# Optimization experiments

Measured on AMD Instinct MI355X. Metric: run time of the kernel, lower is better.

The kernel has to match this reference:

```python
import jax, jax.numpy as jnp
import numpy as np

B, T, D = 2, 2048, 1024
H, HD = 16, 64  # num_heads, num_hiddens_per_head


def setup_inputs() -> dict:
    key = jax.random.key(0)
    ks = jax.random.split(key, 6)
    scale = 1.0 / np.sqrt(D)
    inputs_q = jax.random.normal(ks[0], (B, T, D), dtype=jnp.float32)
    inputs_kv = jax.random.normal(ks[1], (B, T, D), dtype=jnp.float32)
    # causal mask, broadcastable to [b, h, t, T]
    mask = jnp.tril(jnp.ones((T, T), dtype=bool))[None, None, :, :]
    Wq = jax.random.normal(ks[2], (D, H * HD), dtype=jnp.float32) * scale
    Wk = jax.random.normal(ks[3], (D, H * HD), dtype=jnp.float32) * scale
    Wv = jax.random.normal(ks[4], (D, H * HD), dtype=jnp.float32) * scale
    Wo = jax.random.normal(ks[5], (H * HD, D), dtype=jnp.float32) * scale
    return {"inputs_q": inputs_q, "inputs_kv": inputs_kv, "mask": mask,
            "Wq": Wq, "Wk": Wk, "Wv": Wv, "Wo": Wo}


def reference(inputs_q, inputs_kv, mask, Wq, Wk, Wv, Wo):
    b, t, _ = inputs_q.shape
    q = (inputs_q @ Wq).reshape(b, -1, H, HD)
    k = (inputs_kv @ Wk).reshape(b, -1, H, HD)
    v = (inputs_kv @ Wv).reshape(b, -1, H, HD)
    scores = jnp.einsum('bthd,bThd->bhtT', q, k) * (1.0 / jnp.sqrt(HD))
    scores = jnp.where(mask, scores, jnp.finfo(jnp.float32).min)
    attn = jax.nn.softmax(scores, axis=-1)
    out = jnp.einsum('bhtT,bThd->bthd', attn, v).reshape(b, t, H * HD)
    return out @ Wo
```

## Files before the change

### kernel.cpp

```cpp
#include <hip/hip_runtime.h>
#include <hip/hip_bf16.h>

#define B_  2
#define T_  2048
#define D_  1024
#define H_  16
#define HD_ 64

typedef __bf16 bf16x8 __attribute__((ext_vector_type(8)));
typedef float  f32x4  __attribute__((ext_vector_type(4)));

#define MFIX 8.0f

__device__ __forceinline__ __bf16 f2b(float f) {
  __hip_bfloat16 h = __float2bfloat16(f);
  return *reinterpret_cast<__bf16*>(&h);
}

__device__ __forceinline__ void gload_lds16(const __bf16* g, __bf16* l) {
  __builtin_amdgcn_global_load_lds((const unsigned int*)g, (unsigned int*)l, 16, 0, 0);
}

__global__ __launch_bounds__(256) void prep_k(const float* __restrict__ Xq,
                                              const float* __restrict__ Xkv,
                                              const float* __restrict__ Wq,
                                              const float* __restrict__ Wk,
                                              const float* __restrict__ Wv,
                                              const float* __restrict__ Wo,
                                              __hip_bfloat16* __restrict__ Xq_b,
                                              __hip_bfloat16* __restrict__ Xkv_b,
                                              __hip_bfloat16* __restrict__ WTall,
                                              __hip_bfloat16* __restrict__ WoT) {
  const int blk = blockIdx.x;
  if (blk < 8192) {
    const float* x = (blk < 4096) ? Xq : Xkv;
    __hip_bfloat16* y = (blk < 4096) ? Xq_b : Xkv_b;
    const size_t i = ((size_t)(blk & 4095) * 256 + threadIdx.x) * 4;
    f32x4 v = *(const f32x4*)(x + i);
    union { ushort4 u; __hip_bfloat16 h[4]; } o;
#pragma unroll
    for (int j = 0; j < 4; ++j) o.h[j] = __float2bfloat16(v[j]);
    *(ushort4*)(y + i) = o.u;
    return;
  }
  __shared__ float tile[64][65];
  const int wid  = (blk - 8192) >> 8;
  const int tid_ = (blk - 8192) & 255;
  const float* in = (wid == 0) ? Wq : (wid == 1) ? Wk : (wid == 2) ? Wv : Wo;
  __hip_bfloat16* out = (wid == 3) ? WoT : (WTall + (size_t)wid * 1024 * D_);
  const int bx = (tid_ & 15) * 64, by = (tid_ >> 4) * 64;
  const int tx = threadIdx.x & 63, ty = threadIdx.x >> 6;
#pragma unroll
  for (int i = ty; i < 64; i += 4)
    tile[i][tx] = in[(size_t)(by + i) * D_ + bx + tx];
  __syncthreads();
#pragma unroll
  for (int i = ty; i < 64; i += 4)
    out[(size_t)(bx + i) * D_ + by + tx] = __float2bfloat16(tile[tx][i]);
}

__global__ __launch_bounds__(256) void vtrans_k(const __hip_bfloat16* __restrict__ in,
                                                __hip_bfloat16* __restrict__ out) {
  __shared__ __hip_bfloat16 tl[64][65];
  const int bh = blockIdx.y;
  const int t0 = blockIdx.x * 64;
  const int tx = threadIdx.x & 63, ty = threadIdx.x >> 6;
  const __hip_bfloat16* src = in + (size_t)bh * T_ * HD_;
  __hip_bfloat16* dst = out + (size_t)bh * HD_ * T_;
#pragma unroll
  for (int i = ty; i < 64; i += 4)
    tl[i][tx] = src[(size_t)(t0 + i) * HD_ + tx];
  __syncthreads();
#pragma unroll
  for (int i = ty; i < 64; i += 4)
    dst[(size_t)i * T_ + t0 + tx] = tl[tx][i];
}

__global__ __launch_bounds__(256) void gemm_qkv_k(const __bf16* __restrict__ Aq,
                                                  const __bf16* __restrict__ Akv,
                                                  const __bf16* __restrict__ WTall,
                                                  __hip_bfloat16* __restrict__ Qd,
                                                  __hip_bfloat16* __restrict__ Kd,
                                                  __hip_bfloat16* __restrict__ Vd) {
  __shared__ __align__(16) __bf16 Al[128 * 32];
  __shared__ __align__(16) __bf16 Bl[128 * 32];

  const int bm = blockIdx.x * 128;
  const int bn = blockIdx.y * 128;
  const int w  = bn >> 10;
  const __bf16* A = (w == 0) ? Aq : Akv;

  const int wave = threadIdx.x >> 6, lane = threadIdx.x & 63;
  const int wm = (wave >> 1) * 64, wn = (wave & 1) * 64;
  const int lo = lane & 15, qh = lane >> 4;

  const int srow = threadIdx.x >> 2;
  const int skc  = (threadIdx.x & 3) * 8;
  const __bf16* Ag0 = A      + (size_t)(bm + srow) * D_ + skc;
  const __bf16* Bg0 = WTall  + (size_t)(bn + srow) * D_ + skc;
  __bf16* Al0 = Al + threadIdx.x * 8;
  __bf16* Bl0 = Bl + threadIdx.x * 8;

  f32x4 acc[4][4] = {};

  for (int k0 = 0; k0 < D_; k0 += 32) {
    __syncthreads();
    gload_lds16(Ag0 + k0,           Al0);
    gload_lds16(Ag0 + 64 * D_ + k0, Al0 + 64 * 32);
    gload_lds16(Bg0 + k0,           Bl0);
    gload_lds16(Bg0 + 64 * D_ + k0, Bl0 + 64 * 32);
    __syncthreads();

    bf16x8 af[4], bfr[4];
#pragma unroll
    for (int mt = 0; mt < 4; ++mt)
      af[mt] = *(const bf16x8*)(Al + (wm + mt * 16 + lo) * 32 + qh * 8);
#pragma unroll
    for (int nt = 0; nt < 4; ++nt)
      bfr[nt] = *(const bf16x8*)(Bl + (wn + nt * 16 + lo) * 32 + qh * 8);
#pragma unroll
    for (int mt = 0; mt < 4; ++mt)
#pragma unroll
      for (int nt = 0; nt < 4; ++nt)
        acc[mt][nt] = __builtin_amdgcn_mfma_f32_16x16x32_bf16(af[mt], bfr[nt], acc[mt][nt], 0, 0, 0);
  }

  __hip_bfloat16* dst = (w == 0) ? Qd : (w == 1) ? Kd : Vd;
  const float scale = (w == 0) ? 0.125f : 1.0f;
  const int col0 = (bn + wn) & 1023;
#pragma unroll
  for (int mt = 0; mt < 4; ++mt)
#pragma unroll
    for (int nt = 0; nt < 4; ++nt)
#pragma unroll
      for (int r = 0; r < 4; ++r) {
        const int m = bm + wm + mt * 16 + 4 * qh + r;
        const int n = col0 + nt * 16 + lo;
        const int b = m >> 11, t = m & (T_ - 1);
        const int h = n >> 6,  d = n & 63;
        dst[(((size_t)(b * H_ + h) * T_ + t) << 6) + d] =
            __float2bfloat16(acc[mt][nt][r] * scale);
      }
}

__global__ __launch_bounds__(256) void gemm_out_k(const __bf16* __restrict__ A,
                                                  const __bf16* __restrict__ Bt,
                                                  float* __restrict__ C) {
  __shared__ __align__(16) __bf16 Al[128 * 32];
  __shared__ __align__(16) __bf16 Bl[64 * 32];

  const int bm = blockIdx.x * 128;
  const int bn = blockIdx.y * 64;
  const int wave = threadIdx.x >> 6, lane = threadIdx.x & 63;
  const int wm = (wave >> 1) * 64, wn = (wave & 1) * 32;
  const int lo = lane & 15, qh = lane >> 4;

  const int srow = threadIdx.x >> 2;
  const int skc  = (threadIdx.x & 3) * 8;
  const __bf16* Ag0 = A  + (size_t)(bm + srow) * D_ + skc;
  const __bf16* Bg0 = Bt + (size_t)(bn + srow) * D_ + skc;
  __bf16* Al0 = Al + threadIdx.x * 8;
  __bf16* Bl0 = Bl + threadIdx.x * 8;

  f32x4 acc[4][2] = {};

  for (int k0 = 0; k0 < D_; k0 += 32) {
    __syncthreads();
    gload_lds16(Ag0 + k0,           Al0);
    gload_lds16(Ag0 + 64 * D_ + k0, Al0 + 64 * 32);
    gload_lds16(Bg0 + k0,           Bl0);
    __syncthreads();

    bf16x8 af[4], bfr[2];
#pragma unroll
    for (int mt = 0; mt < 4; ++mt)
      af[mt] = *(const bf16x8*)(Al + (wm + mt * 16 + lo) * 32 + qh * 8);
#pragma unroll
    for (int nt = 0; nt < 2; ++nt)
      bfr[nt] = *(const bf16x8*)(Bl + (wn + nt * 16 + lo) * 32 + qh * 8);
#pragma unroll
    for (int mt = 0; mt < 4; ++mt)
#pragma unroll
      for (int nt = 0; nt < 2; ++nt)
        acc[mt][nt] = __builtin_amdgcn_mfma_f32_16x16x32_bf16(af[mt], bfr[nt], acc[mt][nt], 0, 0, 0);
  }

#pragma unroll
  for (int mt = 0; mt < 4; ++mt)
#pragma unroll
    for (int nt = 0; nt < 2; ++nt)
#pragma unroll
      for (int r = 0; r < 4; ++r) {
        const int m = bm + wm + mt * 16 + 4 * qh + r;
        const int n = bn + wn + nt * 16 + lo;
        C[(size_t)m * D_ + n] = acc[mt][nt][r];
      }
}

__global__ __launch_bounds__(256) void attn_slice_k(const __hip_bfloat16* __restrict__ Q,
                                                    const __hip_bfloat16* __restrict__ K,
                                                    const __hip_bfloat16* __restrict__ Vt,
                                                    float* __restrict__ Ppart) {
  __shared__ __align__(16) __bf16 Kl[64 * 64];
  __shared__ __align__(16) __bf16 Vl[64 * 64];
  __shared__ __align__(16) __bf16 Pl[4][16][72];

  const int bh = blockIdx.x;
  const int u  = blockIdx.y;
  int qb, sl;
  if (u < 8)       { qb = u;                    sl = 0; }
  else if (u < 24) { qb = 8  + ((u - 8) >> 1);  sl = (u - 8) & 1; }
  else if (u < 48) { qb = 16 + (u - 24) / 3;    sl = (u - 24) % 3; }
  else             { qb = 24 + ((u - 48) >> 2); sl = (u - 48) & 3; }
  const int jt0 = sl * 8;
  const int jt_end = (jt0 + 8 < qb + 1) ? jt0 + 8 : qb + 1;
  const int t0 = qb * 64;

  const int wave = threadIdx.x >> 6, lane = threadIdx.x & 63;
  const int lo = lane & 15, qh = lane >> 4;

  const __hip_bfloat16* Qb = Q  + (size_t)bh * T_ * HD_;
  const __bf16* Kb = (const __bf16*)(K  + (size_t)bh * T_ * HD_);
  const __bf16* Vb = (const __bf16*)(Vt + (size_t)bh * HD_ * T_);

  const int srow = threadIdx.x >> 3;
  const int ssc  = (threadIdx.x & 7) ^ (srow & 7);
  __bf16* Kd0 = Kl + threadIdx.x * 8;
  __bf16* Kd1 = Kl + 2048 + threadIdx.x * 8;
  __bf16* Vd0 = Vl + threadIdx.x * 8;
  __bf16* Vd1 = Vl + 2048 + threadIdx.x * 8;

  bf16x8 qf[2];
  qf[0] = *(const bf16x8*)(Qb + (size_t)(t0 + wave * 16 + lo) * HD_ + qh * 8);
  qf[1] = *(const bf16x8*)(Qb + (size_t)(t0 + wave * 16 + lo) * HD_ + 32 + qh * 8);

  const int rc0 = (qh)     ^ (lo & 7);
  const int rc1 = (4 + qh) ^ (lo & 7);

  f32x4 o[4] = {};
  float lp[4] = {0.f, 0.f, 0.f, 0.f};

  for (int jt = jt0; jt < jt_end; ++jt) {
    const int jb = jt * 64;
    const bool diag = (jt == qb);

    __syncthreads();
    gload_lds16(Kb + (size_t)(jb + srow)      * HD_ + ssc * 8, Kd0);
    gload_lds16(Kb + (size_t)(jb + 32 + srow) * HD_ + ssc * 8, Kd1);
    gload_lds16(Vb + (size_t)srow        * T_ + jb + ssc * 8, Vd0);
    gload_lds16(Vb + (size_t)(32 + srow) * T_ + jb + ssc * 8, Vd1);
    __syncthreads();

    f32x4 s[4];
#pragma unroll
    for (int nt = 0; nt < 4; ++nt) {
      if (diag && nt > wave) { s[nt] = (f32x4){-1e30f, -1e30f, -1e30f, -1e30f}; continue; }
      f32x4 acc = {0.f, 0.f, 0.f, 0.f};
      bf16x8 kf0 = *(const bf16x8*)(Kl + (nt * 16 + lo) * 64 + rc0 * 8);
      acc = __builtin_amdgcn_mfma_f32_16x16x32_bf16(qf[0], kf0, acc, 0, 0, 0);
      bf16x8 kf1 = *(const bf16x8*)(Kl + (nt * 16 + lo) * 64 + rc1 * 8);
      acc = __builtin_amdgcn_mfma_f32_16x16x32_bf16(qf[1], kf1, acc, 0, 0, 0);
      if (diag && nt == wave) {
#pragma unroll
        for (int r = 0; r < 4; ++r)
          if (lo > 4 * qh + r) acc[r] = -1e30f;
      }
      s[nt] = acc;
    }

#pragma unroll
    for (int nt = 0; nt < 4; ++nt)
#pragma unroll
      for (int r = 0; r < 4; ++r) {
        const float p = __expf(s[nt][r] - MFIX);
        lp[r] += p;
        Pl[wave][4 * qh + r][nt * 16 + lo] = f2b(p);
      }

#pragma unroll
    for (int ks = 0; ks < 2; ++ks) {
      bf16x8 pf = *(const bf16x8*)&Pl[wave][lo][ks * 32 + qh * 8];
      const int rc = ks ? rc1 : rc0;
#pragma unroll
      for (int nt = 0; nt < 4; ++nt) {
        bf16x8 vf = *(const bf16x8*)(Vl + (nt * 16 + lo) * 64 + rc * 8);
        o[nt] = __builtin_amdgcn_mfma_f32_16x16x32_bf16(pf, vf, o[nt], 0, 0, 0);
      }
    }
  }

#pragma unroll
  for (int r = 0; r < 4; ++r)
#pragma unroll
    for (int msk = 1; msk < 16; msk <<= 1)
      lp[r] += __shfl_xor(lp[r], msk, 64);

  float* base = Ppart + (size_t)(bh * 80 + u) * 64 * 65 + (size_t)wave * 16 * 65;
#pragma unroll
  for (int nt = 0; nt < 4; ++nt)
#pragma unroll
    for (int r = 0; r < 4; ++r)
      base[(4 * qh + r) * 65 + nt * 16 + lo] = o[nt][r];
  if (lo == 0) {
#pragma unroll
    for (int r = 0; r < 4; ++r)
      base[(4 * qh + r) * 65 + 64] = lp[r];
  }
}

__global__ __launch_bounds__(256) void attn_combine_k(const float* __restrict__ Ppart,
                                                      __hip_bfloat16* __restrict__ O) {
  const int bh = blockIdx.x, qb = blockIdx.y;
  const int ns = (qb >> 3) + 1;
  const int ubase = (qb < 8) ? qb
                  : (qb < 16) ? 8 + 2 * (qb - 8)
                  : (qb < 24) ? 24 + 3 * (qb - 16)
                  : 48 + 4 * (qb - 24);
  const int d = threadIdx.x & 63, r0 = threadIdx.x >> 6;
  const int b = bh >> 4, h = bh & 15;
  const float* ub = Ppart + (size_t)(bh * 80 + ubase) * 64 * 65;

  for (int row = r0; row < 64; row += 4) {
    float acc = 0.f, l = 0.f;
    for (int s = 0; s < ns; ++s) {
      acc += ub[(size_t)s * 64 * 65 + row * 65 + d];
      l   += ub[(size_t)s * 64 * 65 + row * 65 + 64];
    }
    const int t = qb * 64 + row;
    O[((size_t)(b * T_ + t) << 10) + h * 64 + d] = __float2bfloat16(acc / l);
  }
}

extern "C" void kernel_launch(void* const* d_in, const int* in_sizes, int n_in,
                              void* d_out, int out_size, void* d_ws, size_t ws_size,
                              hipStream_t stream) {
  const float* Xq  = (const float*)d_in[0];
  const float* Xkv = (const float*)d_in[1];
  const float* Wq  = (const float*)d_in[3];
  const float* Wk  = (const float*)d_in[4];
  const float* Wv  = (const float*)d_in[5];
  const float* Wo  = (const float*)d_in[6];

  char* ws = (char*)d_ws;
  const size_t MB = 1024ull * 1024ull;
  __hip_bfloat16* WTall = (__hip_bfloat16*)(ws + 0 * MB);
  __hip_bfloat16* WoT   = (__hip_bfloat16*)(ws + 6 * MB);
  __hip_bfloat16* Qw    = (__hip_bfloat16*)(ws + 8 * MB);
  __hip_bfloat16* Kw    = (__hip_bfloat16*)(ws + 16 * MB);
  __hip_bfloat16* Vw    = (__hip_bfloat16*)(ws + 24 * MB);
  __hip_bfloat16* AO    = (__hip_bfloat16*)(ws + 32 * MB);
  float*          Ppart = (float*)        (ws + 40 * MB);
  __hip_bfloat16* Xq_b  = (__hip_bfloat16*)(ws + 84 * MB);
  __hip_bfloat16* Xkv_b = (__hip_bfloat16*)(ws + 92 * MB);

  const dim3 tb(256);

  prep_k<<<dim3(9216), tb, 0, stream>>>(Xq, Xkv, Wq, Wk, Wv, Wo,
                                        Xq_b, Xkv_b, WTall, WoT);

  gemm_qkv_k<<<dim3(32, 24), tb, 0, stream>>>((const __bf16*)Xq_b, (const __bf16*)Xkv_b,
                                              (const __bf16*)WTall, Qw, Kw, AO);

  vtrans_k<<<dim3(32, 32), tb, 0, stream>>>(AO, Vw);

  attn_slice_k<<<dim3(B_ * H_, 80), tb, 0, stream>>>(Qw, Kw, Vw, Ppart);
  attn_combine_k<<<dim3(B_ * H_, T_ / 64), tb, 0, stream>>>(Ppart, AO);

  gemm_out_k<<<dim3(32, 16), tb, 0, stream>>>((const __bf16*)AO, (const __bf16*)WoT,
                                              (float*)d_out);
}
```

Baseline: 233.2 us.

## Fuse V transpose into QKV GEMM epilogue and shrink attention partials

Moves the V transpose into the QKV GEMM epilogue using an LDS staging tile, which removes the separate vtrans kernel and its extra round trip through global memory. Attention query blocks that need only one slice now normalize and write their output directly, so the combine kernel only handles the remaining 24 query blocks. Partial outputs are stored as bf16 with separate float row sums, which roughly halves partial-sum traffic at the cost of some precision in the split-K combine. The V epilogue adds two extra barriers and LDS use in the GEMM.

```diff
diff --git a/kernel.cpp b/kernel.cpp
--- a/kernel.cpp
+++ b/kernel.cpp
@@ -59,23 +59,6 @@
     out[(size_t)(bx + i) * D_ + by + tx] = __float2bfloat16(tile[tx][i]);
 }
 
-__global__ __launch_bounds__(256) void vtrans_k(const __hip_bfloat16* __restrict__ in,
-                                                __hip_bfloat16* __restrict__ out) {
-  __shared__ __hip_bfloat16 tl[64][65];
-  const int bh = blockIdx.y;
-  const int t0 = blockIdx.x * 64;
-  const int tx = threadIdx.x & 63, ty = threadIdx.x >> 6;
-  const __hip_bfloat16* src = in + (size_t)bh * T_ * HD_;
-  __hip_bfloat16* dst = out + (size_t)bh * HD_ * T_;
-#pragma unroll
-  for (int i = ty; i < 64; i += 4)
-    tl[i][tx] = src[(size_t)(t0 + i) * HD_ + tx];
-  __syncthreads();
-#pragma unroll
-  for (int i = ty; i < 64; i += 4)
-    dst[(size_t)i * T_ + t0 + tx] = tl[tx][i];
-}
-
 __global__ __launch_bounds__(256) void gemm_qkv_k(const __bf16* __restrict__ Aq,
                                                   const __bf16* __restrict__ Akv,
                                                   const __bf16* __restrict__ WTall,
@@ -84,6 +67,7 @@
                                                   __hip_bfloat16* __restrict__ Vd) {
   __shared__ __align__(16) __bf16 Al[128 * 32];
   __shared__ __align__(16) __bf16 Bl[128 * 32];
+  __shared__ __align__(16) __bf16 Tr[64][136];
 
   const int bm = blockIdx.x * 128;
   const int bn = blockIdx.y * 128;
@@ -125,22 +109,48 @@
         acc[mt][nt] = __builtin_amdgcn_mfma_f32_16x16x32_bf16(af[mt], bfr[nt], acc[mt][nt], 0, 0, 0);
   }
 
-  __hip_bfloat16* dst = (w == 0) ? Qd : (w == 1) ? Kd : Vd;
-  const float scale = (w == 0) ? 0.125f : 1.0f;
-  const int col0 = (bn + wn) & 1023;
-#pragma unroll
-  for (int mt = 0; mt < 4; ++mt)
-#pragma unroll
-    for (int nt = 0; nt < 4; ++nt)
-#pragma unroll
-      for (int r = 0; r < 4; ++r) {
-        const int m = bm + wm + mt * 16 + 4 * qh + r;
-        const int n = col0 + nt * 16 + lo;
-        const int b = m >> 11, t = m & (T_ - 1);
-        const int h = n >> 6,  d = n & 63;
-        dst[(((size_t)(b * H_ + h) * T_ + t) << 6) + d] =
-            __float2bfloat16(acc[mt][nt][r] * scale);
-      }
+  if (w == 2) {
+    const int bV  = bm >> 11;
+    const int tV0 = bm & (T_ - 1);
+#pragma unroll
+    for (int ph = 0; ph < 2; ++ph) {
+      __syncthreads();
+      if ((wn >> 6) == ph) {
+#pragma unroll
+        for (int mt = 0; mt < 4; ++mt)
+#pragma unroll
+          for (int nt = 0; nt < 4; ++nt)
+#pragma unroll
+            for (int r = 0; r < 4; ++r)
+              Tr[nt * 16 + lo][wm + mt * 16 + 4 * qh + r] = f2b(acc[mt][nt][r]);
+      }
+      __syncthreads();
+      const int hcol = ((bn & 1023) >> 6) + ph;
+      const int row  = threadIdx.x >> 2;
+      const int tc   = (threadIdx.x & 3) * 32;
+      __hip_bfloat16* dst = Vd + (((size_t)(bV * H_ + hcol) * HD_ + row) * T_) + tV0 + tc;
+#pragma unroll
+      for (int j = 0; j < 32; j += 8)
+        *(bf16x8*)(__bf16*)(dst + j) = *(const bf16x8*)&Tr[row][tc + j];
+    }
+  } else {
+    __hip_bfloat16* dst = (w == 0) ? Qd : Kd;
+    const float scale = (w == 0) ? 0.125f : 1.0f;
+    const int col0 = (bn + wn) & 1023;
+#pragma unroll
+    for (int mt = 0; mt < 4; ++mt)
+#pragma unroll
+      for (int nt = 0; nt < 4; ++nt)
+#pragma unroll
+        for (int r = 0; r < 4; ++r) {
+          const int m = bm + wm + mt * 16 + 4 * qh + r;
+          const int n = col0 + nt * 16 + lo;
+          const int b = m >> 11, t = m & (T_ - 1);
+          const int h = n >> 6,  d = n & 63;
+          dst[(((size_t)(b * H_ + h) * T_ + t) << 6) + d] =
+              __float2bfloat16(acc[mt][nt][r] * scale);
+        }
+  }
 }
 
 __global__ __launch_bounds__(256) void gemm_out_k(const __bf16* __restrict__ A,
@@ -200,7 +210,9 @@
 __global__ __launch_bounds__(256) void attn_slice_k(const __hip_bfloat16* __restrict__ Q,
                                                     const __hip_bfloat16* __restrict__ K,
                                                     const __hip_bfloat16* __restrict__ Vt,
-                                                    float* __restrict__ Ppart) {
+                                                    __hip_bfloat16* __restrict__ Po,
+                                                    float* __restrict__ Lp,
+                                                    __hip_bfloat16* __restrict__ AO) {
   __shared__ __align__(16) __bf16 Kl[64 * 64];
   __shared__ __align__(16) __bf16 Vl[64 * 64];
   __shared__ __align__(16) __bf16 Pl[4][16][72];
@@ -295,36 +307,49 @@
     for (int msk = 1; msk < 16; msk <<= 1)
       lp[r] += __shfl_xor(lp[r], msk, 64);
 
-  float* base = Ppart + (size_t)(bh * 80 + u) * 64 * 65 + (size_t)wave * 16 * 65;
-#pragma unroll
-  for (int nt = 0; nt < 4; ++nt)
-#pragma unroll
-    for (int r = 0; r < 4; ++r)
-      base[(4 * qh + r) * 65 + nt * 16 + lo] = o[nt][r];
-  if (lo == 0) {
-#pragma unroll
-    for (int r = 0; r < 4; ++r)
-      base[(4 * qh + r) * 65 + 64] = lp[r];
-  }
-}
-
-__global__ __launch_bounds__(256) void attn_combine_k(const float* __restrict__ Ppart,
+  if (u < 8) {
+    const int b = bh >> 4, h = bh & 15;
+#pragma unroll
+    for (int nt = 0; nt < 4; ++nt)
+#pragma unroll
+      for (int r = 0; r < 4; ++r) {
+        const int q = t0 + wave * 16 + 4 * qh + r;
+        AO[((size_t)(b * T_ + q) << 10) + h * 64 + nt * 16 + lo] =
+            __float2bfloat16(o[nt][r] / lp[r]);
+      }
+  } else {
+    __hip_bfloat16* base = Po + (size_t)(bh * 80 + u) * 4096 + (size_t)wave * 16 * 64;
+#pragma unroll
+    for (int nt = 0; nt < 4; ++nt)
+#pragma unroll
+      for (int r = 0; r < 4; ++r)
+        base[(4 * qh + r) * 64 + nt * 16 + lo] = __float2bfloat16(o[nt][r]);
+    if (lo == 0) {
+#pragma unroll
+      for (int r = 0; r < 4; ++r)
+        Lp[(size_t)(bh * 80 + u) * 64 + wave * 16 + 4 * qh + r] = lp[r];
+    }
+  }
+}
+
+__global__ __launch_bounds__(256) void attn_combine_k(const __hip_bfloat16* __restrict__ Po,
+                                                      const float* __restrict__ Lp,
                                                       __hip_bfloat16* __restrict__ O) {
-  const int bh = blockIdx.x, qb = blockIdx.y;
+  const int bh = blockIdx.x, qb = 8 + blockIdx.y;
   const int ns = (qb >> 3) + 1;
-  const int ubase = (qb < 8) ? qb
-                  : (qb < 16) ? 8 + 2 * (qb - 8)
+  const int ubase = (qb < 16) ? 8 + 2 * (qb - 8)
                   : (qb < 24) ? 24 + 3 * (qb - 16)
                   : 48 + 4 * (qb - 24);
   const int d = threadIdx.x & 63, r0 = threadIdx.x >> 6;
   const int b = bh >> 4, h = bh & 15;
-  const float* ub = Ppart + (size_t)(bh * 80 + ubase) * 64 * 65;
+  const __hip_bfloat16* ub = Po + (size_t)(bh * 80 + ubase) * 4096;
+  const float* lb = Lp + (size_t)(bh * 80 + ubase) * 64;
 
   for (int row = r0; row < 64; row += 4) {
     float acc = 0.f, l = 0.f;
     for (int s = 0; s < ns; ++s) {
-      acc += ub[(size_t)s * 64 * 65 + row * 65 + d];
-      l   += ub[(size_t)s * 64 * 65 + row * 65 + 64];
+      acc += __bfloat162float(ub[(size_t)s * 4096 + row * 64 + d]);
+      l   += lb[(size_t)s * 64 + row];
     }
     const int t = qb * 64 + row;
     O[((size_t)(b * T_ + t) << 10) + h * 64 + d] = __float2bfloat16(acc / l);
@@ -349,7 +374,8 @@
   __hip_bfloat16* Kw    = (__hip_bfloat16*)(ws + 16 * MB);
   __hip_bfloat16* Vw    = (__hip_bfloat16*)(ws + 24 * MB);
   __hip_bfloat16* AO    = (__hip_bfloat16*)(ws + 32 * MB);
-  float*          Ppart = (float*)        (ws + 40 * MB);
+  __hip_bfloat16* Po    = (__hip_bfloat16*)(ws + 40 * MB);
+  float*          Lpart = (float*)        (ws + 62 * MB);
   __hip_bfloat16* Xq_b  = (__hip_bfloat16*)(ws + 84 * MB);
   __hip_bfloat16* Xkv_b = (__hip_bfloat16*)(ws + 92 * MB);
 
@@ -359,12 +385,10 @@
                                         Xq_b, Xkv_b, WTall, WoT);
 
   gemm_qkv_k<<<dim3(32, 24), tb, 0, stream>>>((const __bf16*)Xq_b, (const __bf16*)Xkv_b,
-                                              (const __bf16*)WTall, Qw, Kw, AO);
-
-  vtrans_k<<<dim3(32, 32), tb, 0, stream>>>(AO, Vw);
-
-  attn_slice_k<<<dim3(B_ * H_, 80), tb, 0, stream>>>(Qw, Kw, Vw, Ppart);
-  attn_combine_k<<<dim3(B_ * H_, T_ / 64), tb, 0, stream>>>(Ppart, AO);
+                                              (const __bf16*)WTall, Qw, Kw, Vw);
+
+  attn_slice_k<<<dim3(B_ * H_, 80), tb, 0, stream>>>(Qw, Kw, Vw, Po, Lpart, AO);
+  attn_combine_k<<<dim3(B_ * H_, 24), tb, 0, stream>>>(Po, Lpart, AO);
 
   gemm_out_k<<<dim3(32, 16), tb, 0, stream>>>((const __bf16*)AO, (const __bf16*)WoT,
                                               (float*)d_out);
```

Result: faster. 225.6 us (-3.3%).
